# Kernel optimization log

Measured on AMD Instinct MI355X. Metric: run time of the kernel, lower is better.

The kernel has to match this reference:

```python
import jax, jax.numpy as jnp
import numpy as np

# Static configuration (uniform ragged layout: every sequence has the same lengths)
B = 8          # number of sequences
QLEN = 256     # new query tokens per sequence
D = 1024       # embedding_dim
H = 16         # num_attention_heads
HD = D // H    # head dim = 64
FFN = 4096     # ffn_embedding_dim
PAGE = 16      # KV-cache page size
KV_TOTAL = 4096            # total KV length per sequence (prefix + new)
P = KV_TOTAL // PAGE       # pages per sequence = 256
NEW_PAGES = QLEN // PAGE   # pages occupied by the new tokens = 16
NUM_PAGES = B * P          # 2048
PREFIX = KV_TOTAL - QLEN   # cached prefix length per sequence
SCALE = HD ** -0.5
LN_EPS = 1e-5


def layer_norm(x, g, b):
    mu = jnp.mean(x, axis=-1, keepdims=True)
    var = jnp.mean(jnp.square(x - mu), axis=-1, keepdims=True)
    return (x - mu) * jax.lax.rsqrt(var + LN_EPS) * g + b


def setup_inputs() -> dict:
    key = jax.random.key(0)
    ks = jax.random.split(key, 12)
    s = 0.02
    inp = {
        "x": jax.random.normal(ks[0], (B * QLEN, D), jnp.float32),
        "pagetable": jax.random.normal(ks[1], (NUM_PAGES, 2, PAGE, H, HD), jnp.float32) * 0.5,
        "Wq": jax.random.normal(ks[2], (D, D), jnp.float32) * s,
        "bq": jnp.zeros((D,), jnp.float32),
        "Wk": jax.random.normal(ks[3], (D, D), jnp.float32) * s,
        "bk": jnp.zeros((D,), jnp.float32),
        "Wv": jax.random.normal(ks[4], (D, D), jnp.float32) * s,
        "bv": jnp.zeros((D,), jnp.float32),
        "Wo": jax.random.normal(ks[5], (D, D), jnp.float32) * s,
        "bo": jnp.zeros((D,), jnp.float32),
        "ln1_g": jnp.ones((D,), jnp.float32),
        "ln1_b": jnp.zeros((D,), jnp.float32),
        "W1": jax.random.normal(ks[6], (D, FFN), jnp.float32) * s,
        "b1": jnp.zeros((FFN,), jnp.float32),
        "W2": jax.random.normal(ks[7], (FFN, D), jnp.float32) * s,
        "b2": jnp.zeros((D,), jnp.float32),
        "lnf_g": jnp.ones((D,), jnp.float32),
        "lnf_b": jnp.zeros((D,), jnp.float32),
        "qo_indptr": jnp.arange(B + 1, dtype=jnp.int32) * QLEN,
        "paged_kv_indptr": jnp.arange(B + 1, dtype=jnp.int32) * P,
        "paged_kv_indices": jnp.arange(NUM_PAGES, dtype=jnp.int32),
        "paged_kv_last_page_len": jnp.full((B,), PAGE, jnp.int32),
        "layer_idx": 0,
    }
    return inp


def reference(x, pagetable, Wq, bq, Wk, bk, Wv, bv, Wo, bo,
              ln1_g, ln1_b, W1, b1, W2, b2, lnf_g, lnf_b,
              qo_indptr, paged_kv_indptr, paged_kv_indices,
              paged_kv_last_page_len, layer_idx):
    residual = x

    # ---- paged self-attention (post-LN path: layer_norm_first=False) ----
    q = ((x @ Wq + bq) * SCALE).reshape(B, QLEN, H, HD)
    k_new = (x @ Wk + bk).reshape(B, QLEN, H, HD)
    v_new = (x @ Wv + bv).reshape(B, QLEN, H, HD)

    # append new K/V into the last NEW_PAGES pages of each sequence
    page_ids = paged_kv_indices.reshape(B, P)                 # [B, P]
    new_ids = page_ids[:, P - NEW_PAGES:].reshape(-1)         # [B*NEW_PAGES]
    kv_new = jnp.stack([k_new, v_new], axis=2)                # [B, QLEN, 2, H, HD]
    kv_new = kv_new.reshape(B, NEW_PAGES, PAGE, 2, H, HD).transpose(0, 1, 3, 2, 4, 5)
    pt = pagetable.at[new_ids].set(kv_new.reshape(-1, 2, PAGE, H, HD))

    # gather the full paged KV per sequence
    kv = pt[page_ids]                                         # [B, P, 2, PAGE, H, HD]
    K = kv[:, :, 0].reshape(B, KV_TOTAL, H, HD)
    V = kv[:, :, 1].reshape(B, KV_TOTAL, H, HD)

    # streaming-causal mask: query i attends to kv positions <= PREFIX + i
    scores = jnp.einsum("bqhd,bkhd->bhqk", q, K)              # [B, H, QLEN, KV_TOTAL]
    kv_pos = jnp.arange(KV_TOTAL)[None, :]
    q_pos = PREFIX + jnp.arange(QLEN)[:, None]
    scores = jnp.where(kv_pos <= q_pos, scores, jnp.float32(-1e30))
    attn = jax.nn.softmax(scores, axis=-1)
    ctx = jnp.einsum("bhqk,bkhd->bqhd", attn, V).reshape(B * QLEN, D)
    x = ctx @ Wo + bo

    x = residual + x
    x = layer_norm(x, ln1_g, ln1_b)

    # ---- FFN ----
    residual = x
    x = jax.nn.relu(x @ W1 + b1)
    x = x @ W2 + b2
    layer_result = x
    x = residual + x
    x = layer_norm(x, lnf_g, lnf_b)

    return x, layer_result, pt
```

## Files before the change

### kernel.cpp

```cpp
#include <hip/hip_runtime.h>
#include <hip/hip_bf16.h>

typedef unsigned short u16;
typedef __attribute__((ext_vector_type(4))) float f32x4;
typedef __attribute__((ext_vector_type(8))) short short8;

#define MODE_QKV 0
#define MODE_WO  1
#define MODE_F1  2
#define MODE_F2  3

__device__ inline u16 f2bf(float f) {
    __hip_bfloat16 h = __float2bfloat16(f);
    return *(u16*)&h;
}

typedef __attribute__((address_space(3))) unsigned int lds_u32_t;
typedef const __attribute__((address_space(1))) unsigned int glb_u32_t;
__device__ inline void gload16(const u16* g, u16* l) {
    __builtin_amdgcn_global_load_lds((glb_u32_t*)(const void*)g,
                                     (lds_u32_t*)(void*)l, 16, 0, 0);
}

__global__ __launch_bounds__(256) void prep_wx(
    const float* __restrict__ Wq, const float* __restrict__ Wk,
    const float* __restrict__ Wv, const float* __restrict__ x,
    u16* __restrict__ WqkvT, u16* __restrict__ xb) {
    int bid = blockIdx.x;
    int tid = threadIdx.x;
    int tx = tid & 31, ty = tid >> 5;
    if (bid >= 3072) {
        int i = (bid - 3072) * 256 + tid;
        const float4* p = (const float4*)(x + (size_t)i * 8);
        float4 a = p[0], b = p[1];
        u16 t[8] = {f2bf(a.x), f2bf(a.y), f2bf(a.z), f2bf(a.w),
                    f2bf(b.x), f2bf(b.y), f2bf(b.z), f2bf(b.w)};
        *(uint4*)(xb + (size_t)i * 8) = *(const uint4*)t;
        return;
    }
    int m = bid >> 10, r = bid & 1023;
    const float* src = (m == 0) ? Wq : (m == 1) ? Wk : Wv;
    u16* dst = WqkvT + (size_t)m * 1024 * 1024;
    __shared__ float t[32][33];
    int n0 = (r & 31) * 32, k0 = (r >> 5) * 32;
#pragma unroll
    for (int j = 0; j < 32; j += 8)
        t[ty + j][tx] = src[(size_t)(k0 + ty + j) * 1024 + n0 + tx];
    __syncthreads();
#pragma unroll
    for (int j = 0; j < 32; j += 8)
        dst[(size_t)(n0 + ty + j) * 1024 + k0 + tx] = f2bf(t[tx][ty + j]);
}

__global__ __launch_bounds__(256) void ln_row(const float* __restrict__ in,
                                              const float* __restrict__ g,
                                              const float* __restrict__ be,
                                              float* __restrict__ outf,
                                              u16* __restrict__ outb) {
    int row = blockIdx.x;
    int tid = threadIdx.x;
    const float* p = in + (size_t)row * 1024 + tid * 4;
    float4 v = *(const float4*)p;
    float s = v.x + v.y + v.z + v.w;
#pragma unroll
    for (int m = 1; m < 64; m <<= 1) s += __shfl_xor(s, m, 64);
    __shared__ float red1[4], red2[4];
    int w = tid >> 6;
    if ((tid & 63) == 0) red1[w] = s;
    __syncthreads();
    float mu = (red1[0] + red1[1] + red1[2] + red1[3]) * (1.0f / 1024.0f);
    float dx = v.x - mu, dy = v.y - mu, dz = v.z - mu, dw = v.w - mu;
    float q = dx * dx + dy * dy + dz * dz + dw * dw;
#pragma unroll
    for (int m = 1; m < 64; m <<= 1) q += __shfl_xor(q, m, 64);
    if ((tid & 63) == 0) red2[w] = q;
    __syncthreads();
    float var = (red2[0] + red2[1] + red2[2] + red2[3]) * (1.0f / 1024.0f);
    float rs = rsqrtf(var + 1e-5f);
    int c = tid * 4;
    float o0 = dx * rs * g[c + 0] + be[c + 0];
    float o1 = dy * rs * g[c + 1] + be[c + 1];
    float o2 = dz * rs * g[c + 2] + be[c + 2];
    float o3 = dw * rs * g[c + 3] + be[c + 3];
    if (outf) {
        float4 o; o.x = o0; o.y = o1; o.z = o2; o.w = o3;
        *(float4*)(outf + (size_t)row * 1024 + c) = o;
    }
    if (outb) {
        u16 t[4] = {f2bf(o0), f2bf(o1), f2bf(o2), f2bf(o3)};
        *(uint2*)&outb[(size_t)row * 1024 + c] = *(const uint2*)t;
    }
}

template <int MODE>
__device__ __forceinline__ void gemm_body(
    u16* As, u16* Bs, int m0, int n0,
    const u16* __restrict__ A, const u16* __restrict__ Bt, int K, int N,
    const float* __restrict__ bias0, const float* __restrict__ bias1,
    const float* __restrict__ bias2, const float* __restrict__ aux,
    float* __restrict__ o0, float* __restrict__ o1, u16* __restrict__ ob,
    u16* __restrict__ kbf, u16* __restrict__ vbf, const int* __restrict__ kvidx) {
    int tid = threadIdx.x;
    int l = tid & 63, w = tid >> 6;
    int wr = w >> 1, wc = w & 1;
    int lr = l & 15, lg = l >> 4;
    int lrow8 = l >> 3;
    int scol = ((l & 7) ^ lrow8) << 3;
    f32x4 acc[4][4] = {};
    for (int kb = 0; kb < K; kb += 64) {
#pragma unroll
        for (int p = 0; p < 4; ++p) {
            int chunk = p * 4 + w;
            int r = chunk * 8 + lrow8;
            gload16(&A[(size_t)(m0 + r) * K + kb + scol], &As[chunk * 512]);
            gload16(&Bt[(size_t)(n0 + r) * K + kb + scol], &Bs[chunk * 512]);
        }
        __syncthreads();
#pragma unroll
        for (int kk = 0; kk < 2; ++kk) {
            short8 a[4], b[4];
            int c0 = kk * 32 + lg * 8;
#pragma unroll
            for (int mi = 0; mi < 4; mi++) {
                int row = wr * 64 + mi * 16 + lr;
                a[mi] = *(const short8*)&As[row * 64 + (c0 ^ ((row & 7) << 3))];
            }
#pragma unroll
            for (int ni = 0; ni < 4; ni++) {
                int row = wc * 64 + ni * 16 + lr;
                b[ni] = *(const short8*)&Bs[row * 64 + (c0 ^ ((row & 7) << 3))];
            }
#pragma unroll
            for (int mi = 0; mi < 4; mi++)
#pragma unroll
                for (int ni = 0; ni < 4; ni++)
                    acc[mi][ni] = __builtin_amdgcn_mfma_f32_16x16x32_bf16(
                        a[mi], b[ni], acc[mi][ni], 0, 0, 0);
        }
        __syncthreads();
    }
#pragma unroll
    for (int mi = 0; mi < 4; mi++) {
#pragma unroll
        for (int ni = 0; ni < 4; ni++) {
#pragma unroll
            for (int r = 0; r < 4; r++) {
                int row = m0 + wr * 64 + mi * 16 + lg * 4 + r;
                int col = n0 + wc * 64 + ni * 16 + lr;
                float v = acc[mi][ni][r];
                if constexpr (MODE == MODE_QKV) {
                    int sel = col >> 10, c = col & 1023;
                    int b = row >> 8, ii = row & 255;
                    int h = (c >> 6), hd = c & 63;
                    if (sel == 0) {
                        ob[(size_t)row * 1024 + c] = f2bf((v + bias0[c]) * 0.125f);
                    } else if (sel == 1) {
                        float val = v + bias1[c];
                        int page = kvidx[b * 256 + 240 + (ii >> 4)];
                        o0[(size_t)page * 32768 + (size_t)(ii & 15) * 1024 + c] = val;
                        kbf[((size_t)(b * 16 + h) * 4096 + 3840 + ii) * 64 + hd] = f2bf(val);
                    } else {
                        float val = v + bias2[c];
                        int page = kvidx[b * 256 + 240 + (ii >> 4)];
                        o0[(size_t)page * 32768 + 16384 + (size_t)(ii & 15) * 1024 + c] = val;
                        vbf[((size_t)(b * 16 + h) * 64 + hd) * 4096 + 3840 + ii] = f2bf(val);
                    }
                } else if constexpr (MODE == MODE_WO) {
                    o0[(size_t)row * N + col] = v + bias0[col] + aux[(size_t)row * N + col];
                } else if constexpr (MODE == MODE_F1) {
                    float t = v + bias0[col];
                    ob[(size_t)row * N + col] = f2bf(fmaxf(t, 0.0f));
                } else {
                    float t = v + bias0[col];
                    o0[(size_t)row * N + col] = t;
                    o1[(size_t)row * N + col] = t + aux[(size_t)row * N + col];
                }
            }
        }
    }
}

template <int MODE>
__global__ __launch_bounds__(256) void gemm_nt(
    const u16* __restrict__ A, const u16* __restrict__ Bt, int K, int N, int gx,
    const float* __restrict__ bias0, const float* __restrict__ aux,
    float* __restrict__ o0, float* __restrict__ o1, u16* __restrict__ ob) {
    __shared__ __align__(16) u16 smem[128 * 64 * 2];
    int bid = blockIdx.x;
    gemm_body<MODE>(smem, smem + 128 * 64, (bid / gx) * 128, (bid % gx) * 128,
                    A, Bt, K, N, bias0, nullptr, nullptr, aux, o0, o1, ob,
                    nullptr, nullptr, nullptr);
}

__global__ __launch_bounds__(256) void qkv_prefix(
    const u16* __restrict__ xb, const u16* __restrict__ WqkvT,
    const float* __restrict__ bq, const float* __restrict__ bk,
    const float* __restrict__ bv,
    float* __restrict__ out_pt, u16* __restrict__ qbuf,
    u16* __restrict__ Kbf, u16* __restrict__ Vtbf,
    const float* __restrict__ pgt, const int* __restrict__ kvidx,
    const float* __restrict__ Wo, const float* __restrict__ W1,
    const float* __restrict__ W2,
    u16* __restrict__ WoT, u16* __restrict__ W1T, u16* __restrict__ W2T) {
    __shared__ __align__(16) u16 smem[128 * 64 * 2];
    int bid = blockIdx.x;
    int tid = threadIdx.x;
    if (bid < 384) {
        gemm_body<MODE_QKV>(smem, smem + 128 * 64, (bid / 24) * 128, (bid % 24) * 128,
                            xb, WqkvT, 1024, 3072, bq, bk, bv, nullptr,
                            out_pt, nullptr, qbuf, Kbf, Vtbf, kvidx);
        return;
    }
    if (bid < 8064) {
        int pbid = bid - 384;
        int tile = pbid % 60, rest = pbid / 60;
        int h = rest & 15, b = rest >> 4;
        int T0 = tile * 64;
        int rr = tid >> 4;
        int hdq = tid & 15;
        u16* vt = smem;
        size_t kdst_base = ((size_t)(b * 16 + h) * 4096 + T0) * 64;
#pragma unroll
        for (int p = 0; p < 4; ++p) {
            int i = p * 16 + rr;
            int page = kvidx[b * 256 + (T0 >> 4) + p];
            size_t src = (size_t)page * 32768 + (size_t)rr * 1024 + h * 64 + hdq * 4;
            float4 kf = *(const float4*)(pgt + src);
            *(float4*)(out_pt + src) = kf;
            u16 kb4[4] = {f2bf(kf.x), f2bf(kf.y), f2bf(kf.z), f2bf(kf.w)};
            *(uint2*)&Kbf[kdst_base + (size_t)i * 64 + hdq * 4] = *(const uint2*)kb4;
            float4 vf = *(const float4*)(pgt + src + 16384);
            *(float4*)(out_pt + src + 16384) = vf;
            u16 vb4[4] = {f2bf(vf.x), f2bf(vf.y), f2bf(vf.z), f2bf(vf.w)};
            *(uint2*)&vt[i * 68 + hdq * 4] = *(const uint2*)vb4;
        }
        __syncthreads();
        size_t vdst_base = (size_t)(b * 16 + h) * 64 * 4096 + T0;
#pragma unroll
        for (int p = 0; p < 4; ++p) {
            int hd = p * 16 + rr;
            u16 o[4];
#pragma unroll
            for (int j = 0; j < 4; ++j) o[j] = vt[(hdq * 4 + j) * 68 + hd];
            *(uint2*)&Vtbf[vdst_base + (size_t)hd * 4096 + hdq * 4] = *(const uint2*)o;
        }
        return;
    }
    int wb = bid - 8064;
    const float* src; u16* dst; int K, N, bx, by;
    if (wb < 1024) {
        bx = wb & 31; by = wb >> 5; K = 1024; N = 1024; src = Wo; dst = WoT;
    } else if (wb < 5120) {
        int r = wb - 1024; bx = r & 127; by = r >> 7; K = 1024; N = 4096; src = W1; dst = W1T;
    } else {
        int r = wb - 5120; bx = r & 31; by = r >> 5; K = 4096; N = 1024; src = W2; dst = W2T;
    }
    float* t = (float*)smem;
    int tx = tid & 31, ty = tid >> 5;
    int n0 = bx * 32, k0 = by * 32;
#pragma unroll
    for (int j = 0; j < 32; j += 8)
        t[(ty + j) * 33 + tx] = src[(size_t)(k0 + ty + j) * N + n0 + tx];
    __syncthreads();
#pragma unroll
    for (int j = 0; j < 32; j += 8)
        dst[(size_t)(n0 + ty + j) * K + k0 + tx] = f2bf(t[tx * 33 + ty + j]);
}

__global__ __launch_bounds__(512) void attn_kernel(const u16* __restrict__ qb,
                                                   const u16* __restrict__ Kbf,
                                                   const u16* __restrict__ Vtbf,
                                                   float* __restrict__ pOct,
                                                   float* __restrict__ pL) {
    __shared__ u16 Ks[64 * 64];
    __shared__ u16 Vt[64 * 64];
    __shared__ u16 Ps[8][16 * 64];
    int bid = blockIdx.x;
    int tid = threadIdx.x;
    int l = tid & 63, w = tid >> 6;
    int lr = l & 15, lg = l >> 4;
    int x = bid & 7, qt = x >> 2, split = x & 3;
    int h = (bid >> 3) & 15, b = bid >> 7;

    int qrow = qt * 128 + w * 16 + lr;
    const u16* qptr = qb + (size_t)(b * 256 + qrow) * 1024 + h * 64 + lg * 8;
    short8 qf0 = *(const short8*)qptr;
    short8 qf1 = *(const short8*)(qptr + 32);

    const u16* kslab = Kbf + (size_t)(b * 16 + h) * 4096 * 64;
    const u16* vslab = Vtbf + (size_t)(b * 16 + h) * 64 * 4096;

    f32x4 octx[4] = {};
    f32x4 lacc = {};
    short8 ones;
#pragma unroll
    for (int j = 0; j < 8; j++) ones[j] = (short)0x3F80;

    int qbase = 3840 + qt * 128;
    int ntiles = (qbase + 128) >> 6;
    int tstart = split * 16;
    int tend = min(tstart + 16, ntiles);
    int kt0 = tstart * 64, kt1 = tend * 64;

    int srow = tid >> 3, scol8 = (tid & 7) * 8;
    int sdst = srow * 64 + (scol8 ^ ((srow & 7) << 3));
    const u16* kp = kslab + srow * 64 + scol8;
    const u16* vp = vslab + (size_t)srow * 4096 + scol8;

    uint4 kreg = *(const uint4*)(kp + (size_t)kt0 * 64);
    uint4 vreg = *(const uint4*)(vp + kt0);
    for (int kt = kt0; kt < kt1; kt += 64) {
        *(uint4*)&Ks[sdst] = kreg;
        *(uint4*)&Vt[sdst] = vreg;
        __syncthreads();
        bool hn = (kt + 64) < kt1;
        if (hn) {
            kreg = *(const uint4*)(kp + (size_t)(kt + 64) * 64);
            vreg = *(const uint4*)(vp + kt + 64);
        }
        float P[4][4];
        bool need_mask = (kt + 63 > qbase);
#pragma unroll
        for (int ni = 0; ni < 4; ni++) {
            f32x4 s = {};
            int krow = ni * 16 + lr;
            int swz = (krow & 7) << 3;
            short8 k0 = *(const short8*)&Ks[krow * 64 + ((lg * 8) ^ swz)];
            short8 k1 = *(const short8*)&Ks[krow * 64 + ((32 + lg * 8) ^ swz)];
            s = __builtin_amdgcn_mfma_f32_16x16x32_bf16(qf0, k0, s, 0, 0, 0);
            s = __builtin_amdgcn_mfma_f32_16x16x32_bf16(qf1, k1, s, 0, 0, 0);
            if (need_mask) {
                int col = kt + ni * 16 + lr;
#pragma unroll
                for (int r = 0; r < 4; r++) {
                    int q = qt * 128 + w * 16 + lg * 4 + r;
                    P[ni][r] = (col <= 3840 + q) ? __expf(s[r]) : 0.0f;
                }
            } else {
#pragma unroll
                for (int r = 0; r < 4; r++) P[ni][r] = __expf(s[r]);
            }
        }
#pragma unroll
        for (int ni = 0; ni < 4; ni++)
#pragma unroll
            for (int r = 0; r < 4; r++) {
                int prow = lg * 4 + r;
                Ps[w][prow * 64 + ((ni * 16 + lr) ^ ((prow & 7) << 3))] = f2bf(P[ni][r]);
            }
#pragma unroll
        for (int kk = 0; kk < 2; kk++) {
            int c0 = kk * 32 + lg * 8;
            short8 pf = *(const short8*)&Ps[w][lr * 64 + (c0 ^ ((lr & 7) << 3))];
            lacc = __builtin_amdgcn_mfma_f32_16x16x32_bf16(pf, ones, lacc, 0, 0, 0);
#pragma unroll
            for (int dt = 0; dt < 4; dt++) {
                int vrow = dt * 16 + lr;
                short8 vf = *(const short8*)&Vt[vrow * 64 + (c0 ^ ((vrow & 7) << 3))];
                octx[dt] = __builtin_amdgcn_mfma_f32_16x16x32_bf16(pf, vf, octx[dt], 0, 0, 0);
            }
        }
        __syncthreads();
    }
    size_t obase = (((size_t)(split * 8 + b) * 16 + h) * 256 + qt * 128) * 64;
#pragma unroll
    for (int dt = 0; dt < 4; dt++)
#pragma unroll
        for (int r = 0; r < 4; r++)
            pOct[obase + (size_t)(w * 16 + lg * 4 + r) * 64 + dt * 16 + lr] = octx[dt][r];
    if (lr == 0) {
        size_t lbase = ((size_t)(split * 8 + b) * 16 + h) * 256 + qt * 128;
#pragma unroll
        for (int r = 0; r < 4; r++) pL[lbase + w * 16 + lg * 4 + r] = lacc[r];
    }
}

__global__ __launch_bounds__(256) void attn_combine(const float* __restrict__ pOct,
                                                    const float* __restrict__ pL,
                                                    u16* __restrict__ ctxb) {
    int row = blockIdx.x;
    int b = row >> 8, q = row & 255;
    int tid = threadIdx.x;
    int h = tid >> 4, dq = (tid & 15) * 4;
    size_t stride = (size_t)128 * 256 * 64;
    size_t base = ((size_t)(b * 16 + h) * 256 + q) * 64 + dq;
    size_t lstride = 128 * 256;
    size_t lbase = (size_t)(b * 16 + h) * 256 + q;
    f32x4 s = {};
    float ls = 0.0f;
#pragma unroll
    for (int sp = 0; sp < 4; sp++) {
        f32x4 v = *(const f32x4*)(pOct + sp * stride + base);
        s += v;
        ls += pL[sp * lstride + lbase];
    }
    float inv = 1.0f / ls;
    u16 o[4] = {f2bf(s[0] * inv), f2bf(s[1] * inv), f2bf(s[2] * inv), f2bf(s[3] * inv)};
    *(uint2*)&ctxb[(size_t)row * 1024 + h * 64 + dq] = *(const uint2*)o;
}

extern "C" void kernel_launch(void* const* d_in, const int* in_sizes, int n_in,
                              void* d_out, int out_size, void* d_ws, size_t ws_size,
                              hipStream_t stream) {
    (void)in_sizes; (void)n_in; (void)out_size; (void)ws_size;
    const float* x   = (const float*)d_in[0];
    const float* pgt = (const float*)d_in[1];
    const float* Wq  = (const float*)d_in[2];
    const float* bq  = (const float*)d_in[3];
    const float* Wk  = (const float*)d_in[4];
    const float* bk  = (const float*)d_in[5];
    const float* Wv  = (const float*)d_in[6];
    const float* bv  = (const float*)d_in[7];
    const float* Wo  = (const float*)d_in[8];
    const float* bo  = (const float*)d_in[9];
    const float* ln1g = (const float*)d_in[10];
    const float* ln1b = (const float*)d_in[11];
    const float* W1  = (const float*)d_in[12];
    const float* b1  = (const float*)d_in[13];
    const float* W2  = (const float*)d_in[14];
    const float* b2  = (const float*)d_in[15];
    const float* lnfg = (const float*)d_in[16];
    const float* lnfb = (const float*)d_in[17];
    const int* kvidx = (const int*)d_in[20];

    float* out = (float*)d_out;
    float* out_x  = out;
    float* out_lr = out + 2048 * 1024;
    float* out_pt = out + 2 * 2048 * 1024;

    char* ws = (char*)d_ws;
    size_t off = 0;
    auto alloc = [&](size_t bytes) { void* p = ws + off; off += (bytes + 255) & ~(size_t)255; return p; };
    u16* WqkvT = (u16*)alloc((size_t)3072 * 1024 * 2);
    u16* WoT   = (u16*)alloc((size_t)1024 * 1024 * 2);
    u16* W1T   = (u16*)alloc((size_t)4096 * 1024 * 2);
    u16* W2T   = (u16*)alloc((size_t)1024 * 4096 * 2);
    u16* xb    = (u16*)alloc((size_t)2048 * 1024 * 2);
    u16* qbuf  = (u16*)alloc((size_t)2048 * 1024 * 2);
    u16* ctxb  = (u16*)alloc((size_t)2048 * 1024 * 2);
    char* regB = (char*)alloc((size_t)2 * 8 * 16 * 4096 * 64 * 2);
    u16* Kbf  = (u16*)regB;
    u16* Vtbf = (u16*)(regB + (size_t)64 * 1024 * 1024);
    float* pOct = (float*)(regB + (size_t)128 * 1024 * 1024);
    float* pL   = (float*)(regB + (size_t)162 * 1024 * 1024);
    float* t1    = (float*)regB;
    float* xln1f = (float*)(regB + (size_t)8 * 1024 * 1024);
    u16*   hb    = (u16*)(regB + (size_t)16 * 1024 * 1024);
    u16*   xln1b = (u16*)(regB + (size_t)32 * 1024 * 1024);
    float* t2 = t1;

    prep_wx<<<4096, 256, 0, stream>>>(Wq, Wk, Wv, x, WqkvT, xb);
    qkv_prefix<<<17280, 256, 0, stream>>>(xb, WqkvT, bq, bk, bv,
                                          out_pt, qbuf, Kbf, Vtbf, pgt, kvidx,
                                          Wo, W1, W2, WoT, W1T, W2T);
    attn_kernel<<<1024, 512, 0, stream>>>(qbuf, Kbf, Vtbf, pOct, pL);
    attn_combine<<<2048, 256, 0, stream>>>(pOct, pL, ctxb);
    gemm_nt<MODE_WO><<<128, 256, 0, stream>>>(ctxb, WoT, 1024, 1024, 8,
        bo, x, t1, nullptr, nullptr);
    ln_row<<<2048, 256, 0, stream>>>(t1, ln1g, ln1b, xln1f, xln1b);
    gemm_nt<MODE_F1><<<512, 256, 0, stream>>>(xln1b, W1T, 1024, 4096, 32,
        b1, nullptr, nullptr, nullptr, hb);
    gemm_nt<MODE_F2><<<128, 256, 0, stream>>>(hb, W2T, 4096, 1024, 8,
        b2, xln1f, out_lr, t2, nullptr);
    ln_row<<<2048, 256, 0, stream>>>(t2, lnfg, lnfb, out_x, nullptr);
}
```

Before: 372.4 us.

## Interleave smaller QKV GEMM tiles with prefix-copy blocks in fused prep kernel

```diff
diff --git a/kernel.cpp b/kernel.cpp
--- a/kernel.cpp
+++ b/kernel.cpp
@@ -96,10 +96,8 @@
 __device__ __forceinline__ void gemm_body(
     u16* As, u16* Bs, int m0, int n0,
     const u16* __restrict__ A, const u16* __restrict__ Bt, int K, int N,
-    const float* __restrict__ bias0, const float* __restrict__ bias1,
-    const float* __restrict__ bias2, const float* __restrict__ aux,
-    float* __restrict__ o0, float* __restrict__ o1, u16* __restrict__ ob,
-    u16* __restrict__ kbf, u16* __restrict__ vbf, const int* __restrict__ kvidx) {
+    const float* __restrict__ bias0, const float* __restrict__ aux,
+    float* __restrict__ o0, float* __restrict__ o1, u16* __restrict__ ob) {
     int tid = threadIdx.x;
     int l = tid & 63, w = tid >> 6;
     int wr = w >> 1, wc = w & 1;
@@ -148,24 +146,7 @@
                 int row = m0 + wr * 64 + mi * 16 + lg * 4 + r;
                 int col = n0 + wc * 64 + ni * 16 + lr;
                 float v = acc[mi][ni][r];
-                if constexpr (MODE == MODE_QKV) {
-                    int sel = col >> 10, c = col & 1023;
-                    int b = row >> 8, ii = row & 255;
-                    int h = (c >> 6), hd = c & 63;
-                    if (sel == 0) {
-                        ob[(size_t)row * 1024 + c] = f2bf((v + bias0[c]) * 0.125f);
-                    } else if (sel == 1) {
-                        float val = v + bias1[c];
-                        int page = kvidx[b * 256 + 240 + (ii >> 4)];
-                        o0[(size_t)page * 32768 + (size_t)(ii & 15) * 1024 + c] = val;
-                        kbf[((size_t)(b * 16 + h) * 4096 + 3840 + ii) * 64 + hd] = f2bf(val);
-                    } else {
-                        float val = v + bias2[c];
-                        int page = kvidx[b * 256 + 240 + (ii >> 4)];
-                        o0[(size_t)page * 32768 + 16384 + (size_t)(ii & 15) * 1024 + c] = val;
-                        vbf[((size_t)(b * 16 + h) * 64 + hd) * 4096 + 3840 + ii] = f2bf(val);
-                    }
-                } else if constexpr (MODE == MODE_WO) {
+                if constexpr (MODE == MODE_WO) {
                     o0[(size_t)row * N + col] = v + bias0[col] + aux[(size_t)row * N + col];
                 } else if constexpr (MODE == MODE_F1) {
                     float t = v + bias0[col];
@@ -188,11 +169,10 @@
     __shared__ __align__(16) u16 smem[128 * 64 * 2];
     int bid = blockIdx.x;
     gemm_body<MODE>(smem, smem + 128 * 64, (bid / gx) * 128, (bid % gx) * 128,
-                    A, Bt, K, N, bias0, nullptr, nullptr, aux, o0, o1, ob,
-                    nullptr, nullptr, nullptr);
-}
-
-__global__ __launch_bounds__(256) void qkv_prefix(
+                    A, Bt, K, N, bias0, aux, o0, o1, ob);
+}
+
+__global__ __launch_bounds__(256, 7) void mega_prep(
     const u16* __restrict__ xb, const u16* __restrict__ WqkvT,
     const float* __restrict__ bq, const float* __restrict__ bk,
     const float* __restrict__ bv,
@@ -202,19 +182,73 @@
     const float* __restrict__ Wo, const float* __restrict__ W1,
     const float* __restrict__ W2,
     u16* __restrict__ WoT, u16* __restrict__ W1T, u16* __restrict__ W2T) {
-    __shared__ __align__(16) u16 smem[128 * 64 * 2];
+    __shared__ __align__(16) u16 smem[64 * 68 * 2];
     int bid = blockIdx.x;
     int tid = threadIdx.x;
-    if (bid < 384) {
-        gemm_body<MODE_QKV>(smem, smem + 128 * 64, (bid / 24) * 128, (bid % 24) * 128,
-                            xb, WqkvT, 1024, 3072, bq, bk, bv, nullptr,
-                            out_pt, nullptr, qbuf, Kbf, Vtbf, kvidx);
+    int rmod = bid % 12, q12 = bid / 12;
+    if (rmod == 0) {
+        u16* As = smem;
+        u16* Bs = smem + 4096;
+        int m0 = (q12 / 48) * 64, n0 = (q12 % 48) * 64;
+        int l = tid & 63, w = tid >> 6;
+        int lr = l & 15, lg = l >> 4;
+        int lrow8 = l >> 3;
+        int scol = ((l & 7) ^ lrow8) << 3;
+        f32x4 acc[4] = {};
+        for (int kb = 0; kb < 1024; kb += 64) {
+#pragma unroll
+            for (int j = 0; j < 2; ++j) {
+                int chunk = w * 2 + j;
+                int r = chunk * 8 + lrow8;
+                gload16(&xb[(size_t)(m0 + r) * 1024 + kb + scol], &As[chunk * 512]);
+                gload16(&WqkvT[(size_t)(n0 + r) * 1024 + kb + scol], &Bs[chunk * 512]);
+            }
+            __syncthreads();
+#pragma unroll
+            for (int kk = 0; kk < 2; ++kk) {
+                int c0 = kk * 32 + lg * 8;
+                int arow = w * 16 + lr;
+                short8 a = *(const short8*)&As[arow * 64 + (c0 ^ ((lr & 7) << 3))];
+#pragma unroll
+                for (int nt = 0; nt < 4; nt++) {
+                    int brow = nt * 16 + lr;
+                    short8 b = *(const short8*)&Bs[brow * 64 + (c0 ^ ((lr & 7) << 3))];
+                    acc[nt] = __builtin_amdgcn_mfma_f32_16x16x32_bf16(a, b, acc[nt], 0, 0, 0);
+                }
+            }
+            __syncthreads();
+        }
+#pragma unroll
+        for (int nt = 0; nt < 4; nt++) {
+#pragma unroll
+            for (int r = 0; r < 4; r++) {
+                int row = m0 + w * 16 + lg * 4 + r;
+                int col = n0 + nt * 16 + lr;
+                float v = acc[nt][r];
+                int sel = col >> 10, c = col & 1023;
+                int b = row >> 8, ii = row & 255;
+                int h = (c >> 6), hd = c & 63;
+                if (sel == 0) {
+                    qbuf[(size_t)row * 1024 + c] = f2bf((v + bq[c]) * 0.125f);
+                } else if (sel == 1) {
+                    float val = v + bk[c];
+                    int page = kvidx[b * 256 + 240 + (ii >> 4)];
+                    out_pt[(size_t)page * 32768 + (size_t)(ii & 15) * 1024 + c] = val;
+                    Kbf[((size_t)(b * 16 + h) * 4096 + 3840 + ii) * 64 + hd] = f2bf(val);
+                } else {
+                    float val = v + bv[c];
+                    int page = kvidx[b * 256 + 240 + (ii >> 4)];
+                    out_pt[(size_t)page * 32768 + 16384 + (size_t)(ii & 15) * 1024 + c] = val;
+                    Vtbf[((size_t)(b * 16 + h) * 64 + hd) * 4096 + 3840 + ii] = f2bf(val);
+                }
+            }
+        }
         return;
     }
-    if (bid < 8064) {
-        int pbid = bid - 384;
-        int tile = pbid % 60, rest = pbid / 60;
-        int h = rest & 15, b = rest >> 4;
+    int rest = q12 * 11 + (rmod - 1);
+    if (rest < 7680) {
+        int tile = rest % 60, rr2 = rest / 60;
+        int h = rr2 & 15, b = rr2 >> 4;
         int T0 = tile * 64;
         int rr = tid >> 4;
         int hdq = tid & 15;
@@ -246,7 +280,7 @@
         }
         return;
     }
-    int wb = bid - 8064;
+    int wb = rest - 7680;
     const float* src; u16* dst; int K, N, bx, by;
     if (wb < 1024) {
         bx = wb & 31; by = wb >> 5; K = 1024; N = 1024; src = Wo; dst = WoT;
@@ -450,9 +484,9 @@
     float* t2 = t1;
 
     prep_wx<<<4096, 256, 0, stream>>>(Wq, Wk, Wv, x, WqkvT, xb);
-    qkv_prefix<<<17280, 256, 0, stream>>>(xb, WqkvT, bq, bk, bv,
-                                          out_pt, qbuf, Kbf, Vtbf, pgt, kvidx,
-                                          Wo, W1, W2, WoT, W1T, W2T);
+    mega_prep<<<18432, 256, 0, stream>>>(xb, WqkvT, bq, bk, bv,
+                                         out_pt, qbuf, Kbf, Vtbf, pgt, kvidx,
+                                         Wo, W1, W2, WoT, W1T, W2T);
     attn_kernel<<<1024, 512, 0, stream>>>(qbuf, Kbf, Vtbf, pOct, pL);
     attn_combine<<<2048, 256, 0, stream>>>(pOct, pL, ctxb);
     gemm_nt<MODE_WO><<<128, 256, 0, stream>>>(ctxb, WoT, 1024, 1024, 8,
```

After: 439.8 us. 18.1% more time.

## Restructure prefix KV conversion per page and move weight transposes into attention launch

Applied to the files above, without the earlier changes.

```diff
diff --git a/kernel.cpp b/kernel.cpp
--- a/kernel.cpp
+++ b/kernel.cpp
@@ -192,91 +192,120 @@
                     nullptr, nullptr, nullptr);
 }
 
-__global__ __launch_bounds__(256) void qkv_prefix(
+__global__ __launch_bounds__(256) void mega_prep(
     const u16* __restrict__ xb, const u16* __restrict__ WqkvT,
     const float* __restrict__ bq, const float* __restrict__ bk,
     const float* __restrict__ bv,
     float* __restrict__ out_pt, u16* __restrict__ qbuf,
     u16* __restrict__ Kbf, u16* __restrict__ Vtbf,
-    const float* __restrict__ pgt, const int* __restrict__ kvidx,
-    const float* __restrict__ Wo, const float* __restrict__ W1,
-    const float* __restrict__ W2,
-    u16* __restrict__ WoT, u16* __restrict__ W1T, u16* __restrict__ W2T) {
-    __shared__ __align__(16) u16 smem[128 * 64 * 2];
+    const float* __restrict__ pgt, const int* __restrict__ kvidx) {
+    __shared__ __align__(16) u16 smem[16640];
     int bid = blockIdx.x;
     int tid = threadIdx.x;
     if (bid < 384) {
-        gemm_body<MODE_QKV>(smem, smem + 128 * 64, (bid / 24) * 128, (bid % 24) * 128,
+        gemm_body<MODE_QKV>(smem, smem + 8192, (bid / 24) * 128, (bid % 24) * 128,
                             xb, WqkvT, 1024, 3072, bq, bk, bv, nullptr,
                             out_pt, nullptr, qbuf, Kbf, Vtbf, kvidx);
         return;
     }
-    if (bid < 8064) {
-        int pbid = bid - 384;
-        int tile = pbid % 60, rest = pbid / 60;
-        int h = rest & 15, b = rest >> 4;
+    if (bid < 864) {
+        int kb2 = bid - 384;
+        int tile = kb2 % 60, b = kb2 / 60;
         int T0 = tile * 64;
-        int rr = tid >> 4;
-        int hdq = tid & 15;
-        u16* vt = smem;
-        size_t kdst_base = ((size_t)(b * 16 + h) * 4096 + T0) * 64;
-#pragma unroll
-        for (int p = 0; p < 4; ++p) {
-            int i = p * 16 + rr;
-            int page = kvidx[b * 256 + (T0 >> 4) + p];
-            size_t src = (size_t)page * 32768 + (size_t)rr * 1024 + h * 64 + hdq * 4;
-            float4 kf = *(const float4*)(pgt + src);
-            *(float4*)(out_pt + src) = kf;
-            u16 kb4[4] = {f2bf(kf.x), f2bf(kf.y), f2bf(kf.z), f2bf(kf.w)};
-            *(uint2*)&Kbf[kdst_base + (size_t)i * 64 + hdq * 4] = *(const uint2*)kb4;
-            float4 vf = *(const float4*)(pgt + src + 16384);
-            *(float4*)(out_pt + src + 16384) = vf;
-            u16 vb4[4] = {f2bf(vf.x), f2bf(vf.y), f2bf(vf.z), f2bf(vf.w)};
-            *(uint2*)&vt[i * 68 + hdq * 4] = *(const uint2*)vb4;
-        }
-        __syncthreads();
-        size_t vdst_base = (size_t)(b * 16 + h) * 64 * 4096 + T0;
-#pragma unroll
-        for (int p = 0; p < 4; ++p) {
-            int hd = p * 16 + rr;
-            u16 o[4];
-#pragma unroll
-            for (int j = 0; j < 4; ++j) o[j] = vt[(hdq * 4 + j) * 68 + hd];
-            *(uint2*)&Vtbf[vdst_base + (size_t)hd * 4096 + hdq * 4] = *(const uint2*)o;
+        int h = tid >> 4, hd0 = (tid & 15) * 4;
+#pragma unroll
+        for (int pi = 0; pi < 4; ++pi) {
+            int page = kvidx[b * 256 + (T0 >> 4) + pi];
+            const float* src = pgt + (size_t)page * 32768;
+            float* dst = out_pt + (size_t)page * 32768;
+            size_t kdst = ((size_t)(b * 16 + h) * 4096 + T0 + pi * 16) * 64 + hd0;
+#pragma unroll
+            for (int it = 0; it < 16; ++it) {
+                size_t o = (size_t)it * 1024 + tid * 4;
+                float4 f = *(const float4*)(src + o);
+                *(float4*)(dst + o) = f;
+                u16 k4[4] = {f2bf(f.x), f2bf(f.y), f2bf(f.z), f2bf(f.w)};
+                *(uint2*)&Kbf[kdst + (size_t)it * 64] = *(const uint2*)k4;
+            }
         }
         return;
     }
-    int wb = bid - 8064;
-    const float* src; u16* dst; int K, N, bx, by;
-    if (wb < 1024) {
-        bx = wb & 31; by = wb >> 5; K = 1024; N = 1024; src = Wo; dst = WoT;
-    } else if (wb < 5120) {
-        int r = wb - 1024; bx = r & 127; by = r >> 7; K = 1024; N = 4096; src = W1; dst = W1T;
-    } else {
-        int r = wb - 5120; bx = r & 31; by = r >> 5; K = 4096; N = 1024; src = W2; dst = W2T;
-    }
-    float* t = (float*)smem;
-    int tx = tid & 31, ty = tid >> 5;
-    int n0 = bx * 32, k0 = by * 32;
-#pragma unroll
-    for (int j = 0; j < 32; j += 8)
-        t[(ty + j) * 33 + tx] = src[(size_t)(k0 + ty + j) * N + n0 + tx];
-    __syncthreads();
-#pragma unroll
-    for (int j = 0; j < 32; j += 8)
-        dst[(size_t)(n0 + ty + j) * K + k0 + tx] = f2bf(t[tx * 33 + ty + j]);
+    int vb2 = bid - 864;
+    int tile = vb2 % 60, b = vb2 / 60;
+    int T0 = tile * 64;
+    int pg[4];
+#pragma unroll
+    for (int pi = 0; pi < 4; ++pi) pg[pi] = kvidx[b * 256 + (T0 >> 4) + pi];
+    u16* vt = smem;
+    int g = tid >> 4, j = tid & 15;
+    for (int hb = 0; hb < 4; ++hb) {
+#pragma unroll
+        for (int it = 0; it < 16; ++it) {
+            int pi = it >> 2;
+            int tokloc = (it & 3) * 4 + (tid >> 6);
+            int ti = pi * 16 + tokloc;
+            int c4 = tid & 63;
+            size_t o = (size_t)pg[pi] * 32768 + 16384 + (size_t)tokloc * 1024
+                       + hb * 256 + c4 * 4;
+            float4 v = *(const float4*)(pgt + o);
+            *(float4*)(out_pt + o) = v;
+            u16 v4[4] = {f2bf(v.x), f2bf(v.y), f2bf(v.z), f2bf(v.w)};
+            *(uint2*)&vt[ti * 260 + c4 * 4] = *(const uint2*)v4;
+        }
+        __syncthreads();
+#pragma unroll
+        for (int rp = 0; rp < 16; ++rp) {
+            int ri = rp * 16 + g;
+            int h = hb * 4 + (ri >> 6), hd = ri & 63;
+            u16 o4[4];
+#pragma unroll
+            for (int s = 0; s < 4; ++s) o4[s] = vt[(j * 4 + s) * 260 + ri];
+            *(uint2*)&Vtbf[((size_t)(b * 16 + h) * 64 + hd) * 4096 + T0 + j * 4] =
+                *(const uint2*)o4;
+        }
+        __syncthreads();
+    }
 }
 
 __global__ __launch_bounds__(512) void attn_kernel(const u16* __restrict__ qb,
                                                    const u16* __restrict__ Kbf,
                                                    const u16* __restrict__ Vtbf,
                                                    float* __restrict__ pOct,
-                                                   float* __restrict__ pL) {
+                                                   float* __restrict__ pL,
+                                                   const float* __restrict__ Wo,
+                                                   const float* __restrict__ W1,
+                                                   const float* __restrict__ W2,
+                                                   u16* __restrict__ WoT,
+                                                   u16* __restrict__ W1T,
+                                                   u16* __restrict__ W2T) {
     __shared__ u16 Ks[64 * 64];
     __shared__ u16 Vt[64 * 64];
     __shared__ u16 Ps[8][16 * 64];
     int bid = blockIdx.x;
     int tid = threadIdx.x;
+    if (bid >= 1024) {
+        int sub = tid >> 8, t2 = tid & 255;
+        int wb = (bid - 1024) * 2 + sub;
+        const float* src; u16* dst; int K, N, bx, by;
+        if (wb < 1024) {
+            bx = wb & 31; by = wb >> 5; K = 1024; N = 1024; src = Wo; dst = WoT;
+        } else if (wb < 5120) {
+            int r = wb - 1024; bx = r & 127; by = r >> 7; K = 1024; N = 4096; src = W1; dst = W1T;
+        } else {
+            int r = wb - 5120; bx = r & 31; by = r >> 5; K = 4096; N = 1024; src = W2; dst = W2T;
+        }
+        float* t = sub ? (float*)Vt : (float*)Ks;
+        int tx = t2 & 31, ty = t2 >> 5;
+        int n0 = bx * 32, k0 = by * 32;
+#pragma unroll
+        for (int jj = 0; jj < 32; jj += 8)
+            t[(ty + jj) * 33 + tx] = src[(size_t)(k0 + ty + jj) * N + n0 + tx];
+        __syncthreads();
+#pragma unroll
+        for (int jj = 0; jj < 32; jj += 8)
+            dst[(size_t)(n0 + ty + jj) * K + k0 + tx] = f2bf(t[tx * 33 + ty + jj]);
+        return;
+    }
     int l = tid & 63, w = tid >> 6;
     int lr = l & 15, lg = l >> 4;
     int x = bid & 7, qt = x >> 2, split = x & 3;
@@ -294,7 +323,7 @@
     f32x4 lacc = {};
     short8 ones;
 #pragma unroll
-    for (int j = 0; j < 8; j++) ones[j] = (short)0x3F80;
+    for (int jj = 0; jj < 8; jj++) ones[jj] = (short)0x3F80;
 
     int qbase = 3840 + qt * 128;
     int ntiles = (qbase + 128) >> 6;
@@ -450,10 +479,10 @@
     float* t2 = t1;
 
     prep_wx<<<4096, 256, 0, stream>>>(Wq, Wk, Wv, x, WqkvT, xb);
-    qkv_prefix<<<17280, 256, 0, stream>>>(xb, WqkvT, bq, bk, bv,
-                                          out_pt, qbuf, Kbf, Vtbf, pgt, kvidx,
+    mega_prep<<<1344, 256, 0, stream>>>(xb, WqkvT, bq, bk, bv,
+                                        out_pt, qbuf, Kbf, Vtbf, pgt, kvidx);
+    attn_kernel<<<5632, 512, 0, stream>>>(qbuf, Kbf, Vtbf, pOct, pL,
                                           Wo, W1, W2, WoT, W1T, W2T);
-    attn_kernel<<<1024, 512, 0, stream>>>(qbuf, Kbf, Vtbf, pOct, pL);
     attn_combine<<<2048, 256, 0, stream>>>(pOct, pL, ctxb);
     gemm_nt<MODE_WO><<<128, 256, 0, stream>>>(ctxb, WoT, 1024, 1024, 8,
         bo, x, t1, nullptr, nullptr);
```

After: 380.3 us. +2.1%, slower.

## Split-K the Wo and FFN2 GEMMs, fuse reductions into layernorm, restructure prefix copy

Applied to the files above, without the earlier changes.

```diff
diff --git a/kernel.cpp b/kernel.cpp
--- a/kernel.cpp
+++ b/kernel.cpp
@@ -52,16 +52,21 @@
         dst[(size_t)(n0 + ty + j) * 1024 + k0 + tx] = f2bf(t[tx][ty + j]);
 }
 
-__global__ __launch_bounds__(256) void ln_row(const float* __restrict__ in,
-                                              const float* __restrict__ g,
-                                              const float* __restrict__ be,
-                                              float* __restrict__ outf,
-                                              u16* __restrict__ outb) {
+__global__ __launch_bounds__(256) void ln_wo(const float* __restrict__ p0,
+                                             const float* __restrict__ p1,
+                                             const float* __restrict__ bo,
+                                             const float* __restrict__ resid,
+                                             const float* __restrict__ g,
+                                             const float* __restrict__ be,
+                                             float* __restrict__ outf,
+                                             u16* __restrict__ outb) {
     int row = blockIdx.x;
     int tid = threadIdx.x;
-    const float* p = in + (size_t)row * 1024 + tid * 4;
-    float4 v = *(const float4*)p;
-    float s = v.x + v.y + v.z + v.w;
+    int c = tid * 4;
+    size_t o = (size_t)row * 1024 + c;
+    f32x4 v = *(const f32x4*)(p0 + o) + *(const f32x4*)(p1 + o)
+            + *(const f32x4*)(bo + c) + *(const f32x4*)(resid + o);
+    float s = v[0] + v[1] + v[2] + v[3];
 #pragma unroll
     for (int m = 1; m < 64; m <<= 1) s += __shfl_xor(s, m, 64);
     __shared__ float red1[4], red2[4];
@@ -69,36 +74,65 @@
     if ((tid & 63) == 0) red1[w] = s;
     __syncthreads();
     float mu = (red1[0] + red1[1] + red1[2] + red1[3]) * (1.0f / 1024.0f);
-    float dx = v.x - mu, dy = v.y - mu, dz = v.z - mu, dw = v.w - mu;
-    float q = dx * dx + dy * dy + dz * dz + dw * dw;
+    f32x4 d = v - mu;
+    float q = d[0] * d[0] + d[1] * d[1] + d[2] * d[2] + d[3] * d[3];
 #pragma unroll
     for (int m = 1; m < 64; m <<= 1) q += __shfl_xor(q, m, 64);
     if ((tid & 63) == 0) red2[w] = q;
     __syncthreads();
     float var = (red2[0] + red2[1] + red2[2] + red2[3]) * (1.0f / 1024.0f);
     float rs = rsqrtf(var + 1e-5f);
+    f32x4 gg = *(const f32x4*)(g + c), bb = *(const f32x4*)(be + c);
+    f32x4 ov = d * rs * gg + bb;
+    *(f32x4*)(outf + o) = ov;
+    u16 t[4] = {f2bf(ov[0]), f2bf(ov[1]), f2bf(ov[2]), f2bf(ov[3])};
+    *(uint2*)&outb[o] = *(const uint2*)t;
+}
+
+__global__ __launch_bounds__(256) void ln_f2(const float* __restrict__ q0,
+                                             const float* __restrict__ b2,
+                                             const float* __restrict__ xln1f,
+                                             const float* __restrict__ g,
+                                             const float* __restrict__ be,
+                                             float* __restrict__ out_lr,
+                                             float* __restrict__ out_x) {
+    int row = blockIdx.x;
+    int tid = threadIdx.x;
     int c = tid * 4;
-    float o0 = dx * rs * g[c + 0] + be[c + 0];
-    float o1 = dy * rs * g[c + 1] + be[c + 1];
-    float o2 = dz * rs * g[c + 2] + be[c + 2];
-    float o3 = dw * rs * g[c + 3] + be[c + 3];
-    if (outf) {
-        float4 o; o.x = o0; o.y = o1; o.z = o2; o.w = o3;
-        *(float4*)(outf + (size_t)row * 1024 + c) = o;
-    }
-    if (outb) {
-        u16 t[4] = {f2bf(o0), f2bf(o1), f2bf(o2), f2bf(o3)};
-        *(uint2*)&outb[(size_t)row * 1024 + c] = *(const uint2*)t;
-    }
+    size_t o = (size_t)row * 1024 + c;
+    const size_t st = (size_t)2048 * 1024;
+    f32x4 v = *(const f32x4*)(q0 + o) + *(const f32x4*)(q0 + st + o)
+            + *(const f32x4*)(q0 + 2 * st + o) + *(const f32x4*)(q0 + 3 * st + o)
+            + *(const f32x4*)(b2 + c);
+    *(f32x4*)(out_lr + o) = v;
+    v = v + *(const f32x4*)(xln1f + o);
+    float s = v[0] + v[1] + v[2] + v[3];
+#pragma unroll
+    for (int m = 1; m < 64; m <<= 1) s += __shfl_xor(s, m, 64);
+    __shared__ float red1[4], red2[4];
+    int w = tid >> 6;
+    if ((tid & 63) == 0) red1[w] = s;
+    __syncthreads();
+    float mu = (red1[0] + red1[1] + red1[2] + red1[3]) * (1.0f / 1024.0f);
+    f32x4 d = v - mu;
+    float q = d[0] * d[0] + d[1] * d[1] + d[2] * d[2] + d[3] * d[3];
+#pragma unroll
+    for (int m = 1; m < 64; m <<= 1) q += __shfl_xor(q, m, 64);
+    if ((tid & 63) == 0) red2[w] = q;
+    __syncthreads();
+    float var = (red2[0] + red2[1] + red2[2] + red2[3]) * (1.0f / 1024.0f);
+    float rs = rsqrtf(var + 1e-5f);
+    f32x4 gg = *(const f32x4*)(g + c), bb = *(const f32x4*)(be + c);
+    *(f32x4*)(out_x + o) = d * rs * gg + bb;
 }
 
 template <int MODE>
 __device__ __forceinline__ void gemm_body(
     u16* As, u16* Bs, int m0, int n0,
-    const u16* __restrict__ A, const u16* __restrict__ Bt, int K, int N,
+    const u16* __restrict__ A, const u16* __restrict__ Bt, int lda, int Kspan, int N,
     const float* __restrict__ bias0, const float* __restrict__ bias1,
-    const float* __restrict__ bias2, const float* __restrict__ aux,
-    float* __restrict__ o0, float* __restrict__ o1, u16* __restrict__ ob,
+    const float* __restrict__ bias2,
+    float* __restrict__ o0, u16* __restrict__ ob,
     u16* __restrict__ kbf, u16* __restrict__ vbf, const int* __restrict__ kvidx) {
     int tid = threadIdx.x;
     int l = tid & 63, w = tid >> 6;
@@ -107,13 +141,13 @@
     int lrow8 = l >> 3;
     int scol = ((l & 7) ^ lrow8) << 3;
     f32x4 acc[4][4] = {};
-    for (int kb = 0; kb < K; kb += 64) {
+    for (int kb = 0; kb < Kspan; kb += 64) {
 #pragma unroll
         for (int p = 0; p < 4; ++p) {
             int chunk = p * 4 + w;
             int r = chunk * 8 + lrow8;
-            gload16(&A[(size_t)(m0 + r) * K + kb + scol], &As[chunk * 512]);
-            gload16(&Bt[(size_t)(n0 + r) * K + kb + scol], &Bs[chunk * 512]);
+            gload16(&A[(size_t)(m0 + r) * lda + kb + scol], &As[chunk * 512]);
+            gload16(&Bt[(size_t)(n0 + r) * lda + kb + scol], &Bs[chunk * 512]);
         }
         __syncthreads();
 #pragma unroll
@@ -165,15 +199,11 @@
                         o0[(size_t)page * 32768 + 16384 + (size_t)(ii & 15) * 1024 + c] = val;
                         vbf[((size_t)(b * 16 + h) * 64 + hd) * 4096 + 3840 + ii] = f2bf(val);
                     }
-                } else if constexpr (MODE == MODE_WO) {
-                    o0[(size_t)row * N + col] = v + bias0[col] + aux[(size_t)row * N + col];
                 } else if constexpr (MODE == MODE_F1) {
                     float t = v + bias0[col];
                     ob[(size_t)row * N + col] = f2bf(fmaxf(t, 0.0f));
                 } else {
-                    float t = v + bias0[col];
-                    o0[(size_t)row * N + col] = t;
-                    o1[(size_t)row * N + col] = t + aux[(size_t)row * N + col];
+                    o0[(size_t)row * N + col] = v;
                 }
             }
         }
@@ -182,17 +212,21 @@
 
 template <int MODE>
 __global__ __launch_bounds__(256) void gemm_nt(
-    const u16* __restrict__ A, const u16* __restrict__ Bt, int K, int N, int gx,
-    const float* __restrict__ bias0, const float* __restrict__ aux,
-    float* __restrict__ o0, float* __restrict__ o1, u16* __restrict__ ob) {
+    const u16* __restrict__ A, const u16* __restrict__ Bt,
+    int lda, int Kspan, int N, int gx, int nper,
+    const float* __restrict__ bias0,
+    float* __restrict__ o0, u16* __restrict__ ob, size_t osplit) {
     __shared__ __align__(16) u16 smem[128 * 64 * 2];
     int bid = blockIdx.x;
-    gemm_body<MODE>(smem, smem + 128 * 64, (bid / gx) * 128, (bid % gx) * 128,
-                    A, Bt, K, N, bias0, nullptr, nullptr, aux, o0, o1, ob,
+    int split = bid / nper, t = bid % nper;
+    gemm_body<MODE>(smem, smem + 128 * 64, (t / gx) * 128, (t % gx) * 128,
+                    A + (size_t)split * Kspan, Bt + (size_t)split * Kspan,
+                    lda, Kspan, N, bias0, nullptr, nullptr,
+                    o0 ? o0 + (size_t)split * osplit : nullptr, ob,
                     nullptr, nullptr, nullptr);
 }
 
-__global__ __launch_bounds__(256) void qkv_prefix(
+__global__ __launch_bounds__(256) void mega_prep(
     const u16* __restrict__ xb, const u16* __restrict__ WqkvT,
     const float* __restrict__ bq, const float* __restrict__ bk,
     const float* __restrict__ bv,
@@ -205,48 +239,72 @@
     __shared__ __align__(16) u16 smem[128 * 64 * 2];
     int bid = blockIdx.x;
     int tid = threadIdx.x;
-    if (bid < 384) {
-        gemm_body<MODE_QKV>(smem, smem + 128 * 64, (bid / 24) * 128, (bid % 24) * 128,
-                            xb, WqkvT, 1024, 3072, bq, bk, bv, nullptr,
-                            out_pt, nullptr, qbuf, Kbf, Vtbf, kvidx);
+    if (bid < 480) {
+        int tile = bid % 60, b = bid / 60;
+        int T0 = tile * 64;
+        int h = tid >> 4, hd0 = (tid & 15) * 4;
+        int pg[4];
+#pragma unroll
+        for (int pi = 0; pi < 4; ++pi) pg[pi] = kvidx[b * 256 + (T0 >> 4) + pi];
+#pragma unroll 4
+        for (int it2 = 0; it2 < 64; ++it2) {
+            int pi = it2 >> 4, it = it2 & 15;
+            const float* src = pgt + (size_t)pg[pi] * 32768;
+            float* dst = out_pt + (size_t)pg[pi] * 32768;
+            size_t o = (size_t)it * 1024 + tid * 4;
+            float4 f = *(const float4*)(src + o);
+            *(float4*)(dst + o) = f;
+            u16 k4[4] = {f2bf(f.x), f2bf(f.y), f2bf(f.z), f2bf(f.w)};
+            size_t kdst = ((size_t)(b * 16 + h) * 4096 + T0 + pi * 16 + it) * 64 + hd0;
+            *(uint2*)&Kbf[kdst] = *(const uint2*)k4;
+        }
         return;
     }
-    if (bid < 8064) {
-        int pbid = bid - 384;
-        int tile = pbid % 60, rest = pbid / 60;
-        int h = rest & 15, b = rest >> 4;
+    if (bid < 960) {
+        int vb2 = bid - 480;
+        int tile = vb2 % 60, b = vb2 / 60;
         int T0 = tile * 64;
-        int rr = tid >> 4;
-        int hdq = tid & 15;
+        int pg[4];
+#pragma unroll
+        for (int pi = 0; pi < 4; ++pi) pg[pi] = kvidx[b * 256 + (T0 >> 4) + pi];
         u16* vt = smem;
-        size_t kdst_base = ((size_t)(b * 16 + h) * 4096 + T0) * 64;
-#pragma unroll
-        for (int p = 0; p < 4; ++p) {
-            int i = p * 16 + rr;
-            int page = kvidx[b * 256 + (T0 >> 4) + p];
-            size_t src = (size_t)page * 32768 + (size_t)rr * 1024 + h * 64 + hdq * 4;
-            float4 kf = *(const float4*)(pgt + src);
-            *(float4*)(out_pt + src) = kf;
-            u16 kb4[4] = {f2bf(kf.x), f2bf(kf.y), f2bf(kf.z), f2bf(kf.w)};
-            *(uint2*)&Kbf[kdst_base + (size_t)i * 64 + hdq * 4] = *(const uint2*)kb4;
-            float4 vf = *(const float4*)(pgt + src + 16384);
-            *(float4*)(out_pt + src + 16384) = vf;
-            u16 vb4[4] = {f2bf(vf.x), f2bf(vf.y), f2bf(vf.z), f2bf(vf.w)};
-            *(uint2*)&vt[i * 68 + hdq * 4] = *(const uint2*)vb4;
-        }
-        __syncthreads();
-        size_t vdst_base = (size_t)(b * 16 + h) * 64 * 4096 + T0;
-#pragma unroll
-        for (int p = 0; p < 4; ++p) {
-            int hd = p * 16 + rr;
-            u16 o[4];
-#pragma unroll
-            for (int j = 0; j < 4; ++j) o[j] = vt[(hdq * 4 + j) * 68 + hd];
-            *(uint2*)&Vtbf[vdst_base + (size_t)hd * 4096 + hdq * 4] = *(const uint2*)o;
+        for (int hb2 = 0; hb2 < 8; ++hb2) {
+#pragma unroll 4
+            for (int it = 0; it < 8; ++it) {
+                int ti = it * 8 + (tid >> 5);
+                int pi = ti >> 4, tokloc = ti & 15;
+                int c4 = (tid & 31) * 4;
+                size_t o = (size_t)pg[pi] * 32768 + 16384 + (size_t)tokloc * 1024
+                           + hb2 * 128 + c4;
+                float4 v = *(const float4*)(pgt + o);
+                *(float4*)(out_pt + o) = v;
+                u16 v4[4] = {f2bf(v.x), f2bf(v.y), f2bf(v.z), f2bf(v.w)};
+                *(uint2*)&vt[ti * 134 + c4] = *(const uint2*)v4;
+            }
+            __syncthreads();
+            int g = tid >> 4, j = tid & 15;
+#pragma unroll
+            for (int rp = 0; rp < 8; ++rp) {
+                int ri = rp * 16 + g;
+                int h = hb2 * 2 + (ri >> 6), hd = ri & 63;
+                u16 o4[4];
+#pragma unroll
+                for (int s = 0; s < 4; ++s) o4[s] = vt[(j * 4 + s) * 134 + ri];
+                *(uint2*)&Vtbf[((size_t)(b * 16 + h) * 64 + hd) * 4096 + T0 + j * 4] =
+                    *(const uint2*)o4;
+            }
+            __syncthreads();
         }
         return;
     }
-    int wb = bid - 8064;
+    if (bid < 1344) {
+        int t = bid - 960;
+        gemm_body<MODE_QKV>(smem, smem + 8192, (t / 24) * 128, (t % 24) * 128,
+                            xb, WqkvT, 1024, 1024, 3072, bq, bk, bv,
+                            out_pt, qbuf, Kbf, Vtbf, kvidx);
+        return;
+    }
+    int wb = bid - 1344;
     const float* src; u16* dst; int K, N, bx, by;
     if (wb < 1024) {
         bx = wb & 31; by = wb >> 5; K = 1024; N = 1024; src = Wo; dst = WoT;
@@ -294,7 +352,7 @@
     f32x4 lacc = {};
     short8 ones;
 #pragma unroll
-    for (int j = 0; j < 8; j++) ones[j] = (short)0x3F80;
+    for (int jj = 0; jj < 8; jj++) ones[jj] = (short)0x3F80;
 
     int qbase = 3840 + qt * 128;
     int ntiles = (qbase + 128) >> 6;
@@ -438,29 +496,30 @@
     u16* xb    = (u16*)alloc((size_t)2048 * 1024 * 2);
     u16* qbuf  = (u16*)alloc((size_t)2048 * 1024 * 2);
     u16* ctxb  = (u16*)alloc((size_t)2048 * 1024 * 2);
-    char* regB = (char*)alloc((size_t)2 * 8 * 16 * 4096 * 64 * 2);
+    char* regB = (char*)alloc((size_t)168 * 1024 * 1024);
     u16* Kbf  = (u16*)regB;
     u16* Vtbf = (u16*)(regB + (size_t)64 * 1024 * 1024);
     float* pOct = (float*)(regB + (size_t)128 * 1024 * 1024);
     float* pL   = (float*)(regB + (size_t)162 * 1024 * 1024);
-    float* t1    = (float*)regB;
-    float* xln1f = (float*)(regB + (size_t)8 * 1024 * 1024);
-    u16*   hb    = (u16*)(regB + (size_t)16 * 1024 * 1024);
-    u16*   xln1b = (u16*)(regB + (size_t)32 * 1024 * 1024);
-    float* t2 = t1;
+    float* p0    = (float*)regB;
+    float* xln1f = (float*)(regB + (size_t)16 * 1024 * 1024);
+    u16*   xln1b = (u16*)(regB + (size_t)24 * 1024 * 1024);
+    u16*   hb    = (u16*)(regB + (size_t)32 * 1024 * 1024);
+    float* q0    = (float*)(regB + (size_t)128 * 1024 * 1024);
 
     prep_wx<<<4096, 256, 0, stream>>>(Wq, Wk, Wv, x, WqkvT, xb);
-    qkv_prefix<<<17280, 256, 0, stream>>>(xb, WqkvT, bq, bk, bv,
-                                          out_pt, qbuf, Kbf, Vtbf, pgt, kvidx,
-                                          Wo, W1, W2, WoT, W1T, W2T);
+    mega_prep<<<10560, 256, 0, stream>>>(xb, WqkvT, bq, bk, bv,
+                                         out_pt, qbuf, Kbf, Vtbf, pgt, kvidx,
+                                         Wo, W1, W2, WoT, W1T, W2T);
     attn_kernel<<<1024, 512, 0, stream>>>(qbuf, Kbf, Vtbf, pOct, pL);
     attn_combine<<<2048, 256, 0, stream>>>(pOct, pL, ctxb);
-    gemm_nt<MODE_WO><<<128, 256, 0, stream>>>(ctxb, WoT, 1024, 1024, 8,
-        bo, x, t1, nullptr, nullptr);
-    ln_row<<<2048, 256, 0, stream>>>(t1, ln1g, ln1b, xln1f, xln1b);
-    gemm_nt<MODE_F1><<<512, 256, 0, stream>>>(xln1b, W1T, 1024, 4096, 32,
-        b1, nullptr, nullptr, nullptr, hb);
-    gemm_nt<MODE_F2><<<128, 256, 0, stream>>>(hb, W2T, 4096, 1024, 8,
-        b2, xln1f, out_lr, t2, nullptr);
-    ln_row<<<2048, 256, 0, stream>>>(t2, lnfg, lnfb, out_x, nullptr);
-}
+    gemm_nt<MODE_WO><<<256, 256, 0, stream>>>(ctxb, WoT, 1024, 512, 1024, 8, 128,
+        nullptr, p0, nullptr, (size_t)2048 * 1024);
+    ln_wo<<<2048, 256, 0, stream>>>(p0, p0 + (size_t)2048 * 1024, bo, x,
+                                    ln1g, ln1b, xln1f, xln1b);
+    gemm_nt<MODE_F1><<<512, 256, 0, stream>>>(xln1b, W1T, 1024, 1024, 4096, 32, 512,
+        b1, nullptr, hb, 0);
+    gemm_nt<MODE_F2><<<512, 256, 0, stream>>>(hb, W2T, 4096, 1024, 1024, 8, 128,
+        nullptr, q0, nullptr, (size_t)2048 * 1024);
+    ln_f2<<<2048, 256, 0, stream>>>(q0, b2, xln1f, lnfg, lnfb, out_lr, out_x);
+}
```

Result: faster. 338.5 us (-9.1%).
